# Performance work log

Hardware: AMD Instinct MI355X
Metric: run time of the kernel (lower is better)

## Reference

```python
import jax, jax.numpy as jnp
import numpy as np

HEADS = 8
EMBED = 64
FEAT_A = 256
FEAT_B = 256


def setup_inputs() -> dict:
    key = jax.random.key(0)
    k1, k2, k3, k4, k5 = jax.random.split(key, 5)
    B, N = 2, 2048
    z_a = jax.random.normal(k1, (B, FEAT_A, N), dtype=jnp.float32)
    z_b = jax.random.normal(k2, (B, FEAT_B, N), dtype=jnp.float32)
    # Conv1d(k=1, bias=False) weights, squeezed: [out_ch, in_ch]
    W_a = jax.random.normal(k3, (HEADS * EMBED, FEAT_A), dtype=jnp.float32) * (1.0 / np.sqrt(FEAT_A))
    W_b = jax.random.normal(k4, (HEADS * EMBED, FEAT_B), dtype=jnp.float32) * (1.0 / np.sqrt(FEAT_B))
    W_c = jax.random.normal(k5, (FEAT_A, HEADS * FEAT_B), dtype=jnp.float32) * (1.0 / np.sqrt(HEADS * FEAT_B))
    return {"z_a": z_a, "z_b": z_b, "W_a": W_a, "W_b": W_b, "W_c": W_c}


def reference(z_a, z_b, W_a, W_b, W_c):
    B, Fa, Na = z_a.shape
    Fb = z_b.shape[1]
    H, E = HEADS, EMBED
    norm = 1.0 / np.sqrt(E)
    # 1x1 conv embeddings -> q, k: [B, H, E, N]
    q = jnp.einsum('of,bfn->bon', W_a, z_a).reshape(B, H, E, Na)
    k = jnp.einsum('of,bfn->bon', W_b, z_b).reshape(B, H, E, -1)
    v = z_b  # [B, Fb, K]
    # coeff_pre_softmax[b,h,q,k] = (q^T k) / sqrt(E)
    pre = jnp.einsum('bheq,bhek->bhqk', q, k) * norm
    coeff = jax.nn.softmax(pre, axis=-1)  # softmax over keys (dim=2 in torch bmm form)
    # l1 loss: mean |pre| over (q,k) per head, averaged over heads
    l1 = jnp.mean(jnp.abs(pre), axis=(1, 2, 3))  # [B]
    # feat[b,h,q,f] = coeff @ v^T
    feat = jnp.einsum('bhqk,bfk->bhqf', coeff, v)
    # combine heads: w[h] = W_c[:, h*Fb:(h+1)*Fb].T  -> [H, Fb, Fa]
    w = W_c.reshape(Fa, H, Fb).transpose(1, 2, 0)
    out = jnp.einsum('bhqf,hfo->bqo', feat, w)  # sum over heads
    return out, l1
```

## Files before the change

kernel.cpp:

```cpp
#include <hip/hip_runtime.h>
#include <hip/hip_bf16.h>


#define B_ 2
#define N_ 2048
#define F_ 256
#define H_ 8
#define E_ 64

typedef __attribute__((ext_vector_type(8))) short bf16x8;
typedef __attribute__((ext_vector_type(4))) float f32x4;

__device__ __forceinline__ unsigned short f2b(float x) {
  __hip_bfloat16 h = __float2bfloat16(x);
  return *reinterpret_cast<unsigned short*>(&h);
}

__device__ __forceinline__ unsigned short f2bt(float x) {
  union { float f; unsigned u; } c; c.f = x;
  return (unsigned short)(c.u >> 16);
}

__device__ __forceinline__ f32x4 mfma16(bf16x8 a, bf16x8 b, f32x4 c) {
  return __builtin_amdgcn_mfma_f32_16x16x32_bf16(a, b, c, 0, 0, 0);
}

__device__ __forceinline__ void async_lds16(const unsigned short* g, unsigned short* l) {
  __builtin_amdgcn_global_load_lds(
      (const __attribute__((address_space(1))) unsigned int*)g,
      (__attribute__((address_space(3))) unsigned int*)l, 16, 0, 0);
}

__global__ __launch_bounds__(256) void prep_kernel(
    const float* __restrict__ W_c, unsigned short* __restrict__ wcb,
    const float* __restrict__ W_a, const float* __restrict__ W_b,
    unsigned short* __restrict__ wab, float* __restrict__ l1acc) {
  int i = blockIdx.x * 256 + threadIdx.x;
  if (i < B_) l1acc[i] = 0.f;
  const int nwc = F_ * H_ * F_ / 4;
  const int nw = 512 * F_ / 4;
  const float* src; unsigned short* dst; int j;
  if (i < nwc) { src = W_c; dst = wcb; j = i; }
  else if (i < nwc + nw) { src = W_a; dst = wab; j = i - nwc; }
  else { j = i - nwc - nw; src = W_b; dst = wab + 512 * F_; }
  float4 v = reinterpret_cast<const float4*>(src)[j];
  unsigned long long pk =
      ((unsigned long long)f2b(v.w) << 48) | ((unsigned long long)f2b(v.z) << 32) |
      ((unsigned long long)f2b(v.y) << 16) | (unsigned long long)f2b(v.x);
  reinterpret_cast<unsigned long long*>(dst)[j] = pk;
}

__global__ __launch_bounds__(256) void transp_kernel(
    const float* __restrict__ z_a, const float* __restrict__ z_b,
    unsigned short* __restrict__ zaT, unsigned short* __restrict__ zbT,
    unsigned short* __restrict__ vbf) {
  __shared__ unsigned int t32[64][65];
  const int tid = threadIdx.x;
  const int nt = blockIdx.x, ft = blockIdx.y, wz = blockIdx.z;
  const int b = wz & 1, which = wz >> 1;
  const float* src = (which ? z_b : z_a) + (size_t)b * F_ * N_;
  unsigned short* dst = (which ? zbT : zaT) + (size_t)b * N_ * F_;
  const int col = tid & 63, rb = tid >> 6;
#pragma unroll
  for (int i = 0; i < 16; ++i) {
    int row = rb + i * 4;
    unsigned short u = f2b(src[(size_t)(ft * 64 + row) * N_ + nt * 64 + col]);
    t32[row][col] = u;
    if (which)
      vbf[(size_t)(b * F_ + ft * 64 + row) * N_ + nt * 64 + col] = u;
  }
  __syncthreads();
#pragma unroll
  for (int i = 0; i < 16; ++i) {
    int row = rb + i * 4;
    dst[(size_t)(nt * 64 + row) * F_ + ft * 64 + col] = (unsigned short)t32[col][row];
  }
}

__global__ __launch_bounds__(256) void proj_mfma(
    const unsigned short* __restrict__ zaT, const unsigned short* __restrict__ zbT,
    const unsigned short* __restrict__ wab,
    unsigned short* __restrict__ qT, unsigned short* __restrict__ kT) {
  __shared__ __align__(16) unsigned short As[64][256];

  const int tid = threadIdx.x;
  const int wid = tid >> 6, lane = tid & 63;
  const int quad = lane >> 4, l16 = lane & 15;
  const int nt = blockIdx.x, ot = blockIdx.y, wz = blockIdx.z;
  const int b = wz & 1, which = wz >> 1;

  const unsigned short* zsrc = (which ? zbT : zaT) + (size_t)b * N_ * F_;
  const unsigned short* wsrc = wab + (size_t)which * 512 * F_;
  unsigned short* dst = (which ? kT : qT) + (size_t)b * N_ * 512;
  const float scale = which ? 1.f : 0.125f;

#pragma unroll
  for (int i = 0; i < 8; ++i) {
    int row = wid * 16 + 2 * i + (lane >> 5);
    int cg = (lane & 31) ^ (row & 31);
    async_lds16(zsrc + (size_t)(nt * 64 + row) * F_ + cg * 8, &As[wid * 16 + 2 * i][0]);
  }

  const unsigned short* brow = wsrc + (size_t)(ot * 64 + wid * 16 + l16) * F_ + quad * 8;

  f32x4 acc[4];
  const f32x4 zero4 = {0.f, 0.f, 0.f, 0.f};
#pragma unroll
  for (int g = 0; g < 4; ++g) acc[g] = zero4;

  __syncthreads();

#pragma unroll
  for (int kt = 0; kt < 8; ++kt) {
    bf16x8 bf = *reinterpret_cast<const bf16x8*>(brow + kt * 32);
#pragma unroll
    for (int g = 0; g < 4; ++g) {
      int row = g * 16 + l16;
      int p = (kt * 4 + quad) ^ (row & 31);
      bf16x8 af = *reinterpret_cast<const bf16x8*>(&As[0][0] + row * 256 + p * 8);
      acc[g] = mfma16(af, bf, acc[g]);
    }
  }

#pragma unroll
  for (int g = 0; g < 4; ++g)
#pragma unroll
    for (int r = 0; r < 4; ++r)
      dst[(size_t)(nt * 64 + g * 16 + quad * 4 + r) * 512 + ot * 64 + wid * 16 + l16] =
          f2b(acc[g][r] * scale);
}

__global__ __launch_bounds__(256, 3) void attn_mfma(
    const unsigned short* __restrict__ qT, const unsigned short* __restrict__ kT,
    const unsigned short* __restrict__ vbf, unsigned short* __restrict__ feat,
    float* __restrict__ l1acc) {
  __shared__ __align__(16) unsigned short ks[2][32][64];
  __shared__ __align__(16) unsigned short vs[2][256][32];
  __shared__ __align__(16) unsigned short p_blk[2][64][40];
  __shared__ float lsum_sh[64];
  __shared__ float redblk[256];

  const int tid = threadIdx.x;
  const int wid = tid >> 6, lane = tid & 63;
  const int quad = lane >> 4, l16 = lane & 15;
  const int qt = blockIdx.x, h = blockIdx.y, b = blockIdx.z;

  const int kkey = wid * 8 + (lane >> 3);
  const int kchunk = (lane & 7) ^ ((kkey >> 1) & 7);
  const unsigned short* kgl =
      kT + ((size_t)(b * N_ + kkey) * 512) + h * 64 + kchunk * 8;
  const unsigned short* vgl[4];
#pragma unroll
  for (int j = 0; j < 4; ++j) {
    int f = (wid * 4 + j) * 16 + (lane >> 2);
    int c = (lane & 3) ^ ((f >> 1) & 3);
    vgl[j] = vbf + ((size_t)(b * F_ + f) * 2048) + c * 8;
  }

  const unsigned short* qrow =
      qT + (size_t)(b * N_ + qt * 64 + wid * 16 + l16) * 512 + h * 64 + quad * 8;
  bf16x8 qf0 = *reinterpret_cast<const bf16x8*>(qrow);
  bf16x8 qf1 = *reinterpret_cast<const bf16x8*>(qrow + 32);

  const int koff = ((quad ^ (l16 & 7)) * 8);
  const int voff = ((quad ^ ((l16 >> 1) & 3)) * 8);

  f32x4 acc[4][4];
  const f32x4 zero4 = {0.f, 0.f, 0.f, 0.f};
#pragma unroll
  for (int g = 0; g < 4; ++g)
#pragma unroll
    for (int t = 0; t < 4; ++t) acc[g][t] = zero4;
  float lsum[4] = {0.f, 0.f, 0.f, 0.f};
  float suml1 = 0.f;
  bf16x8 vreg[4];

  async_lds16(kgl, &ks[0][wid * 8][0]);
#pragma unroll
  for (int j = 0; j < 4; ++j) async_lds16(vgl[j], &vs[0][(wid * 4 + j) * 16][0]);
  __syncthreads();

#pragma unroll 2
  for (int kt = 0; kt < N_ / 32; ++kt) {
    const int cur = kt & 1;
    if (kt + 1 < N_ / 32) {
      async_lds16(kgl + (size_t)(kt + 1) * 32 * 512, &ks[cur ^ 1][wid * 8][0]);
#pragma unroll
      for (int j = 0; j < 4; ++j)
        async_lds16(vgl[j] + (kt + 1) * 32, &vs[cur ^ 1][(wid * 4 + j) * 16][0]);
    }

    const unsigned short* ksc = &ks[cur][0][0];
    bf16x8 kf00 = *reinterpret_cast<const bf16x8*>(ksc + (2 * l16) * 64 + koff);
    bf16x8 kf01 = *reinterpret_cast<const bf16x8*>(ksc + (2 * l16) * 64 + (koff ^ 32));
    bf16x8 kf10 = *reinterpret_cast<const bf16x8*>(ksc + (2 * l16 + 1) * 64 + koff);
    bf16x8 kf11 = *reinterpret_cast<const bf16x8*>(ksc + (2 * l16 + 1) * 64 + (koff ^ 32));

    f32x4 s0 = mfma16(qf0, kf00, zero4); s0 = mfma16(qf1, kf01, s0);
    f32x4 s1 = mfma16(qf0, kf10, zero4); s1 = mfma16(qf1, kf11, s1);

#pragma unroll
    for (int r = 0; r < 4; ++r) {
      float a0 = s0[r], a1 = s1[r];
      suml1 += fabsf(a0) + fabsf(a1);
      float p0 = __expf(a0), p1 = __expf(a1);
      lsum[r] += p0 + p1;
      unsigned pk = ((unsigned)f2bt(p1) << 16) | f2bt(p0);
      *reinterpret_cast<unsigned*>(&p_blk[cur][wid * 16 + quad * 4 + r][2 * l16]) = pk;
    }

    if (kt > 0) {
#pragma unroll
      for (int g = 0; g < 4; ++g) {
        bf16x8 pf = *reinterpret_cast<const bf16x8*>(&p_blk[cur ^ 1][g * 16 + l16][quad * 8]);
#pragma unroll
        for (int t = 0; t < 4; ++t) acc[g][t] = mfma16(pf, vreg[t], acc[g][t]);
      }
    }

    {
      const unsigned short* vsc = &vs[cur][0][0];
#pragma unroll
      for (int t = 0; t < 4; ++t) {
        int f = wid * 64 + t * 16 + l16;
        vreg[t] = *reinterpret_cast<const bf16x8*>(vsc + f * 32 + voff);
      }
    }
    __syncthreads();
  }

  {
#pragma unroll
    for (int g = 0; g < 4; ++g) {
      bf16x8 pf = *reinterpret_cast<const bf16x8*>(&p_blk[1][g * 16 + l16][quad * 8]);
#pragma unroll
      for (int t = 0; t < 4; ++t) acc[g][t] = mfma16(pf, vreg[t], acc[g][t]);
    }
  }

#pragma unroll
  for (int r = 0; r < 4; ++r) {
    float rs = lsum[r];
    rs += __shfl_xor(rs, 1);
    rs += __shfl_xor(rs, 2);
    rs += __shfl_xor(rs, 4);
    rs += __shfl_xor(rs, 8);
    if (l16 == 0) lsum_sh[wid * 16 + quad * 4 + r] = rs;
  }
  __syncthreads();

#pragma unroll
  for (int g = 0; g < 4; ++g)
#pragma unroll
    for (int r = 0; r < 4; ++r) {
      float invl = 1.f / lsum_sh[g * 16 + quad * 4 + r];
      unsigned short* fr =
          feat + (size_t)(b * N_ + qt * 64 + g * 16 + quad * 4 + r) * 2048 +
          h * 256 + wid * 64 + l16;
#pragma unroll
      for (int t = 0; t < 4; ++t) fr[t * 16] = f2b(acc[g][t][r] * invl);
    }

  redblk[tid] = suml1;
  __syncthreads();
  for (int st = 128; st > 0; st >>= 1) {
    if (tid < st) redblk[tid] += redblk[tid + st];
    __syncthreads();
  }
  if (tid == 0) atomicAdd(&l1acc[b], redblk[0]);
}

__global__ __launch_bounds__(256) void combine_mfma(
    const unsigned short* __restrict__ feat, const unsigned short* __restrict__ wcb,
    const float* __restrict__ l1acc, float* __restrict__ out) {
  __shared__ __align__(16) unsigned short As[2][64][256];

  const int tid = threadIdx.x;
  const int wid = tid >> 6, lane = tid & 63;
  const int quad = lane >> 4, l16 = lane & 15;
  const int mb = blockIdx.x, ob = blockIdx.y;

  const int srow_hi = lane >> 5;
  const int spos = lane & 31;

  const unsigned short* brow = wcb + (size_t)(ob * 64 + wid * 16 + l16) * 2048 + quad * 8;

  f32x4 acc[4];
  const f32x4 zero4 = {0.f, 0.f, 0.f, 0.f};
#pragma unroll
  for (int g = 0; g < 4; ++g) acc[g] = zero4;

#pragma unroll
  for (int i = 0; i < 8; ++i) {
    int row = wid * 16 + 2 * i + srow_hi;
    int cg = spos ^ (row & 31);
    async_lds16(feat + (size_t)(mb * 64 + row) * 2048 + cg * 8, &As[0][wid * 16 + 2 * i][0]);
  }
  __syncthreads();

  for (int ch = 0; ch < 8; ++ch) {
    const int cur = ch & 1;
    if (ch + 1 < 8) {
#pragma unroll
      for (int i = 0; i < 8; ++i) {
        int row = wid * 16 + 2 * i + srow_hi;
        int cg = spos ^ (row & 31);
        async_lds16(feat + (size_t)(mb * 64 + row) * 2048 + (ch + 1) * 256 + cg * 8,
                    &As[cur ^ 1][wid * 16 + 2 * i][0]);
      }
    }
#pragma unroll
    for (int kt = 0; kt < 8; ++kt) {
      bf16x8 bf = *reinterpret_cast<const bf16x8*>(brow + ch * 256 + kt * 32);
#pragma unroll
      for (int g = 0; g < 4; ++g) {
        int row = g * 16 + l16;
        int p = (kt * 4 + quad) ^ (row & 31);
        bf16x8 af = *reinterpret_cast<const bf16x8*>(&As[cur][0][0] + row * 256 + p * 8);
        acc[g] = mfma16(af, bf, acc[g]);
      }
    }
    __syncthreads();
  }

#pragma unroll
  for (int g = 0; g < 4; ++g)
#pragma unroll
    for (int r = 0; r < 4; ++r)
      out[(size_t)(mb * 64 + g * 16 + quad * 4 + r) * 256 + ob * 64 + wid * 16 + l16] =
          acc[g][r];

  if (mb == 0 && ob == 0 && tid < B_)
    out[(size_t)B_ * N_ * F_ + tid] = l1acc[tid] * (1.f / (float)(H_ * N_ * N_));
}

extern "C" void kernel_launch(void* const* d_in, const int* in_sizes, int n_in,
                              void* d_out, int out_size, void* d_ws, size_t ws_size,
                              hipStream_t stream) {
  const float* z_a = (const float*)d_in[0];
  const float* z_b = (const float*)d_in[1];
  const float* W_a = (const float*)d_in[2];
  const float* W_b = (const float*)d_in[3];
  const float* W_c = (const float*)d_in[4];
  float* out = (float*)d_out;

  char* ws = (char*)d_ws;
  unsigned short* qT = (unsigned short*)ws;
  unsigned short* kT = (unsigned short*)(ws + ((size_t)4 << 20));
  unsigned short* vbf = (unsigned short*)(ws + ((size_t)8 << 20));
  unsigned short* wcb = (unsigned short*)(ws + ((size_t)10 << 20));
  unsigned short* zaT = (unsigned short*)(ws + ((size_t)11 << 20));
  unsigned short* zbT = (unsigned short*)(ws + ((size_t)13 << 20));
  unsigned short* wab = (unsigned short*)(ws + ((size_t)15 << 20));
  float* l1acc = (float*)(ws + ((size_t)15 << 20) + (768 << 10));
  unsigned short* feat = (unsigned short*)(ws + ((size_t)16 << 20));

  const int nprep = F_ * H_ * F_ / 4 + 2 * (512 * F_ / 4);
  prep_kernel<<<dim3(nprep / 256), 256, 0, stream>>>(
      W_c, wcb, W_a, W_b, wab, l1acc);
  transp_kernel<<<dim3(N_ / 64, F_ / 64, 4), 256, 0, stream>>>(z_a, z_b, zaT, zbT, vbf);
  proj_mfma<<<dim3(N_ / 64, 8, 4), 256, 0, stream>>>(zaT, zbT, wab, qT, kT);
  attn_mfma<<<dim3(N_ / 64, H_, B_), 256, 0, stream>>>(qT, kT, vbf, feat, l1acc);
  combine_mfma<<<dim3(B_ * N_ / 64, 4), 256, 0, stream>>>(feat, wcb, l1acc, out);
}
```

Baseline: 168.0 us.

## Split-K combine GEMM with atomic accumulation and fold weight prep into transpose

The combine GEMM is re-tiled to 32-row blocks that each handle a 512-wide K slice for all 256 output columns. Partial sums are accumulated into the output with float atomicAdd, and the output is zeroed beforehand. The separate weight-conversion kernel is merged into the transpose kernel through a grid-stride loop, which also zeroes the output and the l1 accumulator, saving one launch. The aim is more blocks and higher occupancy for the combine stage, at the cost of atomic traffic, an extra output-zeroing pass, and nondeterministic summation order.

```diff
diff --git a/kernel.cpp b/kernel.cpp
--- a/kernel.cpp
+++ b/kernel.cpp
@@ -31,32 +31,40 @@
       (__attribute__((address_space(3))) unsigned int*)l, 16, 0, 0);
 }
 
-__global__ __launch_bounds__(256) void prep_kernel(
-    const float* __restrict__ W_c, unsigned short* __restrict__ wcb,
-    const float* __restrict__ W_a, const float* __restrict__ W_b,
-    unsigned short* __restrict__ wab, float* __restrict__ l1acc) {
-  int i = blockIdx.x * 256 + threadIdx.x;
-  if (i < B_) l1acc[i] = 0.f;
-  const int nwc = F_ * H_ * F_ / 4;
-  const int nw = 512 * F_ / 4;
-  const float* src; unsigned short* dst; int j;
-  if (i < nwc) { src = W_c; dst = wcb; j = i; }
-  else if (i < nwc + nw) { src = W_a; dst = wab; j = i - nwc; }
-  else { j = i - nwc - nw; src = W_b; dst = wab + 512 * F_; }
-  float4 v = reinterpret_cast<const float4*>(src)[j];
-  unsigned long long pk =
-      ((unsigned long long)f2b(v.w) << 48) | ((unsigned long long)f2b(v.z) << 32) |
-      ((unsigned long long)f2b(v.y) << 16) | (unsigned long long)f2b(v.x);
-  reinterpret_cast<unsigned long long*>(dst)[j] = pk;
-}
-
 __global__ __launch_bounds__(256) void transp_kernel(
     const float* __restrict__ z_a, const float* __restrict__ z_b,
     unsigned short* __restrict__ zaT, unsigned short* __restrict__ zbT,
-    unsigned short* __restrict__ vbf) {
+    unsigned short* __restrict__ vbf,
+    const float* __restrict__ W_c, unsigned short* __restrict__ wcb,
+    const float* __restrict__ W_a, const float* __restrict__ W_b,
+    unsigned short* __restrict__ wab, float* __restrict__ l1acc,
+    float* __restrict__ out) {
   __shared__ unsigned int t32[64][65];
   const int tid = threadIdx.x;
   const int nt = blockIdx.x, ft = blockIdx.y, wz = blockIdx.z;
+
+  {
+    const int NT = 32 * 4 * 4 * 256;
+    int gtid = ((wz * 4 + ft) * 32 + nt) * 256 + tid;
+    if (gtid < B_) l1acc[gtid] = 0.f;
+    const float4 z4 = {0.f, 0.f, 0.f, 0.f};
+    for (int j = gtid; j < B_ * N_ * F_ / 4; j += NT)
+      reinterpret_cast<float4*>(out)[j] = z4;
+    const int nwc = F_ * H_ * F_ / 4;
+    const int nw = 512 * F_ / 4;
+    for (int j0 = gtid; j0 < nwc + 2 * nw; j0 += NT) {
+      const float* src; unsigned short* dst; int j;
+      if (j0 < nwc) { src = W_c; dst = wcb; j = j0; }
+      else if (j0 < nwc + nw) { src = W_a; dst = wab; j = j0 - nwc; }
+      else { src = W_b; dst = wab + 512 * F_; j = j0 - nwc - nw; }
+      float4 v = reinterpret_cast<const float4*>(src)[j];
+      unsigned long long pk =
+          ((unsigned long long)f2b(v.w) << 48) | ((unsigned long long)f2b(v.z) << 32) |
+          ((unsigned long long)f2b(v.y) << 16) | (unsigned long long)f2b(v.x);
+      reinterpret_cast<unsigned long long*>(dst)[j] = pk;
+    }
+  }
+
   const int b = wz & 1, which = wz >> 1;
   const float* src = (which ? z_b : z_a) + (size_t)b * F_ * N_;
   unsigned short* dst = (which ? zbT : zaT) + (size_t)b * N_ * F_;
@@ -273,64 +281,74 @@
 __global__ __launch_bounds__(256) void combine_mfma(
     const unsigned short* __restrict__ feat, const unsigned short* __restrict__ wcb,
     const float* __restrict__ l1acc, float* __restrict__ out) {
-  __shared__ __align__(16) unsigned short As[2][64][256];
+  __shared__ __align__(16) unsigned short As[2][32][256];
 
   const int tid = threadIdx.x;
   const int wid = tid >> 6, lane = tid & 63;
   const int quad = lane >> 4, l16 = lane & 15;
-  const int mb = blockIdx.x, ob = blockIdx.y;
+  const int mb = blockIdx.x, kq = blockIdx.y;
+  const size_t kbase = (size_t)kq * 512;
 
   const int srow_hi = lane >> 5;
   const int spos = lane & 31;
 
-  const unsigned short* brow = wcb + (size_t)(ob * 64 + wid * 16 + l16) * 2048 + quad * 8;
-
-  f32x4 acc[4];
+  f32x4 acc[4][2];
   const f32x4 zero4 = {0.f, 0.f, 0.f, 0.f};
 #pragma unroll
-  for (int g = 0; g < 4; ++g) acc[g] = zero4;
-
-#pragma unroll
-  for (int i = 0; i < 8; ++i) {
-    int row = wid * 16 + 2 * i + srow_hi;
+  for (int ot = 0; ot < 4; ++ot)
+#pragma unroll
+    for (int g = 0; g < 2; ++g) acc[ot][g] = zero4;
+
+#pragma unroll
+  for (int i = 0; i < 4; ++i) {
+    int row = wid * 8 + 2 * i + srow_hi;
     int cg = spos ^ (row & 31);
-    async_lds16(feat + (size_t)(mb * 64 + row) * 2048 + cg * 8, &As[0][wid * 16 + 2 * i][0]);
-  }
-  __syncthreads();
-
-  for (int ch = 0; ch < 8; ++ch) {
-    const int cur = ch & 1;
-    if (ch + 1 < 8) {
-#pragma unroll
-      for (int i = 0; i < 8; ++i) {
-        int row = wid * 16 + 2 * i + srow_hi;
-        int cg = spos ^ (row & 31);
-        async_lds16(feat + (size_t)(mb * 64 + row) * 2048 + (ch + 1) * 256 + cg * 8,
-                    &As[cur ^ 1][wid * 16 + 2 * i][0]);
+    async_lds16(feat + (size_t)(mb * 32 + row) * 2048 + kbase + cg * 8,
+                &As[0][wid * 8 + 2 * i][0]);
+  }
+  __syncthreads();
+
+#pragma unroll
+  for (int i = 0; i < 4; ++i) {
+    int row = wid * 8 + 2 * i + srow_hi;
+    int cg = spos ^ (row & 31);
+    async_lds16(feat + (size_t)(mb * 32 + row) * 2048 + kbase + 256 + cg * 8,
+                &As[1][wid * 8 + 2 * i][0]);
+  }
+
+#pragma unroll
+  for (int ch = 0; ch < 2; ++ch) {
+    if (ch == 1) __syncthreads();
+#pragma unroll
+    for (int kt = 0; kt < 8; ++kt) {
+      int c = kt * 4 + quad;
+      int row0 = l16, row1 = 16 + l16;
+      bf16x8 af0 = *reinterpret_cast<const bf16x8*>(
+          &As[ch][0][0] + row0 * 256 + (c ^ row0) * 8);
+      bf16x8 af1 = *reinterpret_cast<const bf16x8*>(
+          &As[ch][0][0] + row1 * 256 + (c ^ row1) * 8);
+#pragma unroll
+      for (int ot = 0; ot < 4; ++ot) {
+        bf16x8 bf = *reinterpret_cast<const bf16x8*>(
+            wcb + (size_t)(wid * 64 + ot * 16 + l16) * 2048 + kbase + ch * 256 +
+            kt * 32 + quad * 8);
+        acc[ot][0] = mfma16(af0, bf, acc[ot][0]);
+        acc[ot][1] = mfma16(af1, bf, acc[ot][1]);
       }
     }
-#pragma unroll
-    for (int kt = 0; kt < 8; ++kt) {
-      bf16x8 bf = *reinterpret_cast<const bf16x8*>(brow + ch * 256 + kt * 32);
-#pragma unroll
-      for (int g = 0; g < 4; ++g) {
-        int row = g * 16 + l16;
-        int p = (kt * 4 + quad) ^ (row & 31);
-        bf16x8 af = *reinterpret_cast<const bf16x8*>(&As[cur][0][0] + row * 256 + p * 8);
-        acc[g] = mfma16(af, bf, acc[g]);
-      }
-    }
-    __syncthreads();
-  }
-
-#pragma unroll
-  for (int g = 0; g < 4; ++g)
-#pragma unroll
-    for (int r = 0; r < 4; ++r)
-      out[(size_t)(mb * 64 + g * 16 + quad * 4 + r) * 256 + ob * 64 + wid * 16 + l16] =
-          acc[g][r];
-
-  if (mb == 0 && ob == 0 && tid < B_)
+  }
+
+#pragma unroll
+  for (int ot = 0; ot < 4; ++ot)
+#pragma unroll
+    for (int g = 0; g < 2; ++g)
+#pragma unroll
+      for (int r = 0; r < 4; ++r)
+        atomicAdd(&out[(size_t)(mb * 32 + g * 16 + quad * 4 + r) * 256 +
+                       wid * 64 + ot * 16 + l16],
+                  acc[ot][g][r]);
+
+  if (mb == 0 && kq == 0 && tid < B_)
     out[(size_t)B_ * N_ * F_ + tid] = l1acc[tid] * (1.f / (float)(H_ * N_ * N_));
 }
 
@@ -355,11 +373,9 @@
   float* l1acc = (float*)(ws + ((size_t)15 << 20) + (768 << 10));
   unsigned short* feat = (unsigned short*)(ws + ((size_t)16 << 20));
 
-  const int nprep = F_ * H_ * F_ / 4 + 2 * (512 * F_ / 4);
-  prep_kernel<<<dim3(nprep / 256), 256, 0, stream>>>(
-      W_c, wcb, W_a, W_b, wab, l1acc);
-  transp_kernel<<<dim3(N_ / 64, F_ / 64, 4), 256, 0, stream>>>(z_a, z_b, zaT, zbT, vbf);
+  transp_kernel<<<dim3(N_ / 64, F_ / 64, 4), 256, 0, stream>>>(
+      z_a, z_b, zaT, zbT, vbf, W_c, wcb, W_a, W_b, wab, l1acc, out);
   proj_mfma<<<dim3(N_ / 64, 8, 4), 256, 0, stream>>>(zaT, zbT, wab, qT, kT);
   attn_mfma<<<dim3(N_ / 64, H_, B_), 256, 0, stream>>>(qT, kT, vbf, feat, l1acc);
-  combine_mfma<<<dim3(B_ * N_ / 64, 4), 256, 0, stream>>>(feat, wcb, l1acc, out);
-}
+  combine_mfma<<<dim3(B_ * N_ / 32, 4), 256, 0, stream>>>(feat, wcb, l1acc, out);
+}
```

New measurement: 172.6 us. 1.03x slower.

## Fuse transpose/bf16 conversion into projection kernel, dropping zaT/zbT intermediates

Applied to the files above, without the earlier changes.

Merges the transpose kernel and the Q/K projection GEMM into one kernel. Each block loads a 32-column tile of z in fp32, converts it to bf16, transposes it into swizzled LDS, and then computes 256 output channels directly from LDS. This removes the zaT/zbT round-trip through global memory and one launch. In exchange, each z tile is reloaded by two blocks (the oh grid dimension), and the grid has fewer, heavier blocks with more sync points.

```diff
diff --git a/kernel.cpp b/kernel.cpp
--- a/kernel.cpp
+++ b/kernel.cpp
@@ -50,84 +50,82 @@
   reinterpret_cast<unsigned long long*>(dst)[j] = pk;
 }
 
-__global__ __launch_bounds__(256) void transp_kernel(
+__global__ __launch_bounds__(256) void fused_tp(
     const float* __restrict__ z_a, const float* __restrict__ z_b,
-    unsigned short* __restrict__ zaT, unsigned short* __restrict__ zbT,
-    unsigned short* __restrict__ vbf) {
-  __shared__ unsigned int t32[64][65];
+    const unsigned short* __restrict__ wab, unsigned short* __restrict__ vbf,
+    unsigned short* __restrict__ qT, unsigned short* __restrict__ kT) {
+  __shared__ unsigned int t32[64][33];
+  __shared__ __align__(16) unsigned short As[32][256];
+
   const int tid = threadIdx.x;
-  const int nt = blockIdx.x, ft = blockIdx.y, wz = blockIdx.z;
+  const int nt = blockIdx.x, oh = blockIdx.y, wz = blockIdx.z;
   const int b = wz & 1, which = wz >> 1;
   const float* src = (which ? z_b : z_a) + (size_t)b * F_ * N_;
-  unsigned short* dst = (which ? zbT : zaT) + (size_t)b * N_ * F_;
-  const int col = tid & 63, rb = tid >> 6;
-#pragma unroll
-  for (int i = 0; i < 16; ++i) {
-    int row = rb + i * 4;
-    unsigned short u = f2b(src[(size_t)(ft * 64 + row) * N_ + nt * 64 + col]);
-    t32[row][col] = u;
-    if (which)
-      vbf[(size_t)(b * F_ + ft * 64 + row) * N_ + nt * 64 + col] = u;
-  }
-  __syncthreads();
-#pragma unroll
-  for (int i = 0; i < 16; ++i) {
-    int row = rb + i * 4;
-    dst[(size_t)(nt * 64 + row) * F_ + ft * 64 + col] = (unsigned short)t32[col][row];
-  }
-}
-
-__global__ __launch_bounds__(256) void proj_mfma(
-    const unsigned short* __restrict__ zaT, const unsigned short* __restrict__ zbT,
-    const unsigned short* __restrict__ wab,
-    unsigned short* __restrict__ qT, unsigned short* __restrict__ kT) {
-  __shared__ __align__(16) unsigned short As[64][256];
-
-  const int tid = threadIdx.x;
+
+  const int n4 = (tid & 7) * 4;
+  const int frow = tid >> 3;
+  const int n_l = tid & 31;
+  const int jb = tid >> 5;
+
+#pragma unroll
+  for (int s = 0; s < 4; ++s) {
+#pragma unroll
+    for (int pass = 0; pass < 2; ++pass) {
+      int f_l = pass * 32 + frow;
+      float4 v = *reinterpret_cast<const float4*>(
+          &src[(size_t)(s * 64 + f_l) * N_ + nt * 32 + n4]);
+      unsigned short u0 = f2b(v.x), u1 = f2b(v.y), u2 = f2b(v.z), u3 = f2b(v.w);
+      t32[f_l][n4] = u0; t32[f_l][n4 + 1] = u1;
+      t32[f_l][n4 + 2] = u2; t32[f_l][n4 + 3] = u3;
+      if (which && oh == 0) {
+        ushort4 pk = {u0, u1, u2, u3};
+        *reinterpret_cast<ushort4*>(
+            &vbf[(size_t)(b * F_ + s * 64 + f_l) * 2048 + nt * 32 + n4]) = pk;
+      }
+    }
+    __syncthreads();
+    {
+      int c = s * 8 + jb;
+      int p = c ^ n_l;
+      unsigned w0 = t32[jb * 8 + 0][n_l] | (t32[jb * 8 + 1][n_l] << 16);
+      unsigned w1 = t32[jb * 8 + 2][n_l] | (t32[jb * 8 + 3][n_l] << 16);
+      unsigned w2 = t32[jb * 8 + 4][n_l] | (t32[jb * 8 + 5][n_l] << 16);
+      unsigned w3 = t32[jb * 8 + 6][n_l] | (t32[jb * 8 + 7][n_l] << 16);
+      uint4 pk = {w0, w1, w2, w3};
+      *reinterpret_cast<uint4*>(&As[n_l][p * 8]) = pk;
+    }
+    __syncthreads();
+  }
+
   const int wid = tid >> 6, lane = tid & 63;
   const int quad = lane >> 4, l16 = lane & 15;
-  const int nt = blockIdx.x, ot = blockIdx.y, wz = blockIdx.z;
-  const int b = wz & 1, which = wz >> 1;
-
-  const unsigned short* zsrc = (which ? zbT : zaT) + (size_t)b * N_ * F_;
   const unsigned short* wsrc = wab + (size_t)which * 512 * F_;
   unsigned short* dst = (which ? kT : qT) + (size_t)b * N_ * 512;
   const float scale = which ? 1.f : 0.125f;
-
-#pragma unroll
-  for (int i = 0; i < 8; ++i) {
-    int row = wid * 16 + 2 * i + (lane >> 5);
-    int cg = (lane & 31) ^ (row & 31);
-    async_lds16(zsrc + (size_t)(nt * 64 + row) * F_ + cg * 8, &As[wid * 16 + 2 * i][0]);
-  }
-
-  const unsigned short* brow = wsrc + (size_t)(ot * 64 + wid * 16 + l16) * F_ + quad * 8;
-
-  f32x4 acc[4];
   const f32x4 zero4 = {0.f, 0.f, 0.f, 0.f};
-#pragma unroll
-  for (int g = 0; g < 4; ++g) acc[g] = zero4;
-
-  __syncthreads();
-
-#pragma unroll
-  for (int kt = 0; kt < 8; ++kt) {
-    bf16x8 bf = *reinterpret_cast<const bf16x8*>(brow + kt * 32);
-#pragma unroll
-    for (int g = 0; g < 4; ++g) {
-      int row = g * 16 + l16;
-      int p = (kt * 4 + quad) ^ (row & 31);
-      bf16x8 af = *reinterpret_cast<const bf16x8*>(&As[0][0] + row * 256 + p * 8);
-      acc[g] = mfma16(af, bf, acc[g]);
-    }
-  }
-
-#pragma unroll
-  for (int g = 0; g < 4; ++g)
-#pragma unroll
-    for (int r = 0; r < 4; ++r)
-      dst[(size_t)(nt * 64 + g * 16 + quad * 4 + r) * 512 + ot * 64 + wid * 16 + l16] =
-          f2b(acc[g][r] * scale);
+
+#pragma unroll
+  for (int ot = 0; ot < 4; ++ot) {
+    const int o = (oh * 4 + ot) * 64 + wid * 16 + l16;
+    const unsigned short* brow = wsrc + (size_t)o * F_ + quad * 8;
+    f32x4 acc0 = zero4, acc1 = zero4;
+#pragma unroll
+    for (int kt = 0; kt < 8; ++kt) {
+      bf16x8 bf = *reinterpret_cast<const bf16x8*>(brow + kt * 32);
+      const int row0 = l16, row1 = 16 + l16;
+      bf16x8 a0 = *reinterpret_cast<const bf16x8*>(
+          &As[0][0] + row0 * 256 + ((kt * 4 + quad) ^ row0) * 8);
+      bf16x8 a1 = *reinterpret_cast<const bf16x8*>(
+          &As[0][0] + row1 * 256 + ((kt * 4 + quad) ^ row1) * 8);
+      acc0 = mfma16(a0, bf, acc0);
+      acc1 = mfma16(a1, bf, acc1);
+    }
+#pragma unroll
+    for (int r = 0; r < 4; ++r) {
+      dst[(size_t)(nt * 32 + quad * 4 + r) * 512 + o] = f2b(acc0[r] * scale);
+      dst[(size_t)(nt * 32 + 16 + quad * 4 + r) * 512 + o] = f2b(acc1[r] * scale);
+    }
+  }
 }
 
 __global__ __launch_bounds__(256, 3) void attn_mfma(
@@ -349,8 +347,6 @@
   unsigned short* kT = (unsigned short*)(ws + ((size_t)4 << 20));
   unsigned short* vbf = (unsigned short*)(ws + ((size_t)8 << 20));
   unsigned short* wcb = (unsigned short*)(ws + ((size_t)10 << 20));
-  unsigned short* zaT = (unsigned short*)(ws + ((size_t)11 << 20));
-  unsigned short* zbT = (unsigned short*)(ws + ((size_t)13 << 20));
   unsigned short* wab = (unsigned short*)(ws + ((size_t)15 << 20));
   float* l1acc = (float*)(ws + ((size_t)15 << 20) + (768 << 10));
   unsigned short* feat = (unsigned short*)(ws + ((size_t)16 << 20));
@@ -358,8 +354,7 @@
   const int nprep = F_ * H_ * F_ / 4 + 2 * (512 * F_ / 4);
   prep_kernel<<<dim3(nprep / 256), 256, 0, stream>>>(
       W_c, wcb, W_a, W_b, wab, l1acc);
-  transp_kernel<<<dim3(N_ / 64, F_ / 64, 4), 256, 0, stream>>>(z_a, z_b, zaT, zbT, vbf);
-  proj_mfma<<<dim3(N_ / 64, 8, 4), 256, 0, stream>>>(zaT, zbT, wab, qT, kT);
+  fused_tp<<<dim3(N_ / 32, 2, 4), 256, 0, stream>>>(z_a, z_b, wab, vbf, qT, kT);
   attn_mfma<<<dim3(N_ / 64, H_, B_), 256, 0, stream>>>(qT, kT, vbf, feat, l1acc);
   combine_mfma<<<dim3(B_ * N_ / 64, 4), 256, 0, stream>>>(feat, wcb, l1acc, out);
 }
```

After: 165.9 us. About the same (-1.3%).
